# Optimization experiments

Hardware: AMD Instinct MI355X
Metric: run time of the kernel (lower is better)

Reference implementation:

```python
import jax, jax.numpy as jnp
import numpy as np

N = 8192
E = 524288
D_IN, D_HID, D_OUT = 3, 16, 16


def setup_inputs() -> dict:
    key = jax.random.key(0)
    ks = jax.random.split(key, 9)
    node_feats = jax.random.normal(ks[0], (N, D_IN), dtype=jnp.float32)
    edge_idx = jax.random.randint(ks[1], (2, E), 0, N, dtype=jnp.int64)
    # GIN epsilon (train_eps=True -> learned scalar, init 0)
    eps = jnp.zeros((), dtype=jnp.float32)
    # MLP params (Kaiming-uniform-ish scale)
    def lin(k, fan_in, fan_out):
        lim = 1.0 / np.sqrt(fan_in)
        kw, kb = jax.random.split(k)
        W = jax.random.uniform(kw, (fan_in, fan_out), minval=-lim, maxval=lim, dtype=jnp.float32)
        b = jax.random.uniform(kb, (fan_out,), minval=-lim, maxval=lim, dtype=jnp.float32)
        return W, b
    W1, b1 = lin(ks[2], D_IN, D_HID)
    W2, b2 = lin(ks[3], D_HID, D_OUT)
    W3, b3 = lin(ks[4], D_OUT, 1)
    return {"node_feats": node_feats, "edge_idx": edge_idx, "eps": eps,
            "W1": W1, "b1": b1, "W2": W2, "b2": b2, "W3": W3, "b3": b3}


def reference(node_feats, edge_idx, eps, W1, b1, W2, b2, W3, b3):
    src, dst = edge_idx[0], edge_idx[1]
    # GIN aggregation: sum over incoming neighbor features (scatter-add at dst)
    agg = jax.ops.segment_sum(node_feats[src], dst, num_segments=N)  # [N, D_IN]
    z = (1.0 + eps) * node_feats + agg
    # 3-layer MLP with ReLU after every Linear
    h = jax.nn.relu(z @ W1 + b1)
    h = jax.nn.relu(h @ W2 + b2)
    h = jax.nn.relu(h @ W3 + b3)  # [N, 1]
    # outer product: [N,1] @ [1,N] -> [N,N]
    edge_feats = h @ h.T
    return edge_feats
```

## Files before the change

### kernel.cpp

```cpp
#include <hip/hip_runtime.h>
#include <hip/hip_bf16.h>

#define NN 8192
#define EE 524288
#define D_IN 3
#define D_HID 16
#define D_OUT 16
#define NAGG (NN * D_IN)
#define SLICES 64
#define QSPLIT 4
#define EPS_SLICE (EE / SLICES)
#define NODES_Q (NN / QSPLIT)
#define LELE (NODES_Q * D_IN)
#define NCHUNK 8

typedef float f32x4 __attribute__((ext_vector_type(4)));

__device__ __forceinline__ float mlp_eval(float z0, float z1, float z2,
        const float* __restrict__ W1, const float* __restrict__ b1,
        const float* __restrict__ W2, const float* __restrict__ b2,
        const float* __restrict__ W3, const float* __restrict__ b3) {
    float h1[D_HID];
#pragma unroll
    for (int j = 0; j < D_HID; ++j) {
        float v = b1[j] + z0 * W1[0 * D_HID + j] + z1 * W1[1 * D_HID + j] + z2 * W1[2 * D_HID + j];
        h1[j] = v > 0.0f ? v : 0.0f;
    }
    float h2[D_OUT];
#pragma unroll
    for (int j = 0; j < D_OUT; ++j) {
        float v = b2[j];
#pragma unroll
        for (int k = 0; k < D_HID; ++k) v += h1[k] * W2[k * D_OUT + j];
        h2[j] = v > 0.0f ? v : 0.0f;
    }
    float v = b3[0];
#pragma unroll
    for (int k = 0; k < D_OUT; ++k) v += h2[k] * W3[k];
    return v > 0.0f ? v : 0.0f;
}

__global__ __launch_bounds__(512) void scatter_priv_kernel(
        const float* __restrict__ nf,
        const int* __restrict__ eidx,
        float* __restrict__ partials) {
    __shared__ float lagg[LELE];
    const int tid = threadIdx.x;
    const int slice = blockIdx.x & (SLICES - 1);
    const int q = blockIdx.x >> 6;
    for (int i = tid; i < LELE; i += 512) lagg[i] = 0.0f;
    __syncthreads();

    const int base = slice * EPS_SLICE;
    const int nlo = q * NODES_Q;
    for (int e = base + tid; e < base + EPS_SLICE; e += 512) {
        int d = eidx[EE + e];
        unsigned dq = (unsigned)(d - nlo);
        if (dq < (unsigned)NODES_Q) {
            int s = eidx[e];
            atomicAdd(&lagg[dq * 3 + 0], nf[s * 3 + 0]);
            atomicAdd(&lagg[dq * 3 + 1], nf[s * 3 + 1]);
            atomicAdd(&lagg[dq * 3 + 2], nf[s * 3 + 2]);
        }
    }
    __syncthreads();

    f32x4* __restrict__ dst = (f32x4*)(partials + (size_t)slice * NAGG + (size_t)nlo * D_IN);
    const f32x4* __restrict__ src = (const f32x4*)lagg;
    for (int i = tid; i < LELE / 4; i += 512) dst[i] = src[i];
}

__global__ __launch_bounds__(256) void reduce_kernel(
        const float* __restrict__ partials,
        float* __restrict__ partials2) {
    const int c4 = blockIdx.x * 256 + threadIdx.x;
    const int chunk = blockIdx.y;
    const f32x4* __restrict__ p = (const f32x4*)partials;
    f32x4 s = {0.0f, 0.0f, 0.0f, 0.0f};
#pragma unroll
    for (int k = 0; k < SLICES / NCHUNK; ++k)
        s += p[(size_t)(chunk * (SLICES / NCHUNK) + k) * (NAGG / 4) + c4];
    ((f32x4*)partials2)[(size_t)chunk * (NAGG / 4) + c4] = s;
}

__global__ __launch_bounds__(256) void mlp_final_kernel(
        const float* __restrict__ partials2,
        const float* __restrict__ nf,
        const float* __restrict__ epsp,
        const float* __restrict__ W1, const float* __restrict__ b1,
        const float* __restrict__ W2, const float* __restrict__ b2,
        const float* __restrict__ W3, const float* __restrict__ b3,
        float* __restrict__ h) {
    int i = blockIdx.x * blockDim.x + threadIdx.x;
    if (i >= NN) return;
    float z[D_IN];
#pragma unroll
    for (int c = 0; c < D_IN; ++c) {
        float s = 0.0f;
#pragma unroll
        for (int k = 0; k < NCHUNK; ++k) s += partials2[(size_t)k * NAGG + i * 3 + c];
        z[c] = s;
    }
    float eps1 = 1.0f + epsp[0];
    float z0 = eps1 * nf[i * 3 + 0] + z[0];
    float z1 = eps1 * nf[i * 3 + 1] + z[1];
    float z2 = eps1 * nf[i * 3 + 2] + z[2];
    h[i] = mlp_eval(z0, z1, z2, W1, b1, W2, b2, W3, b3);
}

__global__ void zero_agg_kernel(float* __restrict__ agg, int n) {
    int i = blockIdx.x * blockDim.x + threadIdx.x;
    if (i < n) agg[i] = 0.0f;
}

__global__ void scatter_atomic_kernel(const float* __restrict__ nf,
                                      const int* __restrict__ eidx,
                                      float* __restrict__ agg) {
    int e = blockIdx.x * blockDim.x + threadIdx.x;
    if (e >= EE) return;
    int s = eidx[e];
    int d = eidx[EE + e];
    atomicAdd(&agg[d * 3 + 0], nf[s * 3 + 0]);
    atomicAdd(&agg[d * 3 + 1], nf[s * 3 + 1]);
    atomicAdd(&agg[d * 3 + 2], nf[s * 3 + 2]);
}

__global__ void mlp_kernel(const float* __restrict__ nf,
                           const float* __restrict__ agg,
                           const float* __restrict__ epsp,
                           const float* __restrict__ W1, const float* __restrict__ b1,
                           const float* __restrict__ W2, const float* __restrict__ b2,
                           const float* __restrict__ W3, const float* __restrict__ b3,
                           float* __restrict__ h) {
    int i = blockIdx.x * blockDim.x + threadIdx.x;
    if (i >= NN) return;
    float eps1 = 1.0f + epsp[0];
    float z0 = eps1 * nf[i * 3 + 0] + agg[i * 3 + 0];
    float z1 = eps1 * nf[i * 3 + 1] + agg[i * 3 + 1];
    float z2 = eps1 * nf[i * 3 + 2] + agg[i * 3 + 2];
    h[i] = mlp_eval(z0, z1, z2, W1, b1, W2, b2, W3, b3);
}

__global__ __launch_bounds__(256) void outer_kernel(const float* __restrict__ h,
                                                    float4* __restrict__ out) {
    int i = blockIdx.x;
    float hi = h[i];
    const float4* __restrict__ h4 = reinterpret_cast<const float4*>(h);
    float4* __restrict__ row = out + (size_t)i * (NN / 4);
#pragma unroll 4
    for (int j = threadIdx.x; j < NN / 4; j += 256) {
        float4 v = h4[j];
        float4 o;
        o.x = hi * v.x; o.y = hi * v.y; o.z = hi * v.z; o.w = hi * v.w;
        row[j] = o;
    }
}

extern "C" void kernel_launch(void* const* d_in, const int* in_sizes, int n_in,
                              void* d_out, int out_size, void* d_ws, size_t ws_size,
                              hipStream_t stream) {
    const float* nf   = (const float*)d_in[0];
    const int*   eidx = (const int*)d_in[1];
    const float* eps  = (const float*)d_in[2];
    const float* W1   = (const float*)d_in[3];
    const float* b1   = (const float*)d_in[4];
    const float* W2   = (const float*)d_in[5];
    const float* b2   = (const float*)d_in[6];
    const float* W3   = (const float*)d_in[7];
    const float* b3   = (const float*)d_in[8];
    float* out = (float*)d_out;

    float* h         = (float*)d_ws;
    float* agg       = h + NN;
    float* partials2 = agg + NAGG;
    float* partials  = partials2 + (size_t)NCHUNK * NAGG;

    size_t need = (size_t)(NN + NAGG + (size_t)NCHUNK * NAGG + (size_t)SLICES * NAGG) * sizeof(float);

    if (ws_size >= need) {
        scatter_priv_kernel<<<SLICES * QSPLIT, 512, 0, stream>>>(nf, eidx, partials);
        dim3 rgrid(NAGG / 4 / 256, NCHUNK);
        reduce_kernel<<<rgrid, 256, 0, stream>>>(partials, partials2);
        mlp_final_kernel<<<NN / 256, 256, 0, stream>>>(partials2, nf, eps, W1, b1, W2, b2, W3, b3, h);
    } else {
        zero_agg_kernel<<<(NAGG + 255) / 256, 256, 0, stream>>>(agg, NAGG);
        scatter_atomic_kernel<<<(EE + 255) / 256, 256, 0, stream>>>(nf, eidx, agg);
        mlp_kernel<<<(NN + 255) / 256, 256, 0, stream>>>(nf, agg, eps, W1, b1, W2, b2, W3, b3, h);
    }
    outer_kernel<<<NN, 256, 0, stream>>>(h, (float4*)out);
}
```

Before: 68.50 us.

## Fuse partial reduction into MLP kernel and widen outer-product rows per block

Replaces the two-stage reduction (reduce_kernel into partials2, then mlp_final_kernel) with one kernel. Each block sums all 64 slice partials for its 256 nodes into shared memory and then evaluates the MLP, which removes one launch and the partials2 round trip. The outer-product kernel now writes 8 rows per 512-thread block and reuses each loaded h vector across those rows, cutting block count and redundant loads of h. The fused reduction runs on only 32 blocks with 192 active reducer threads each, so that stage has much less parallelism than before.

```diff
diff --git a/kernel.cpp b/kernel.cpp
--- a/kernel.cpp
+++ b/kernel.cpp
@@ -12,7 +12,8 @@
 #define EPS_SLICE (EE / SLICES)
 #define NODES_Q (NN / QSPLIT)
 #define LELE (NODES_Q * D_IN)
-#define NCHUNK 8
+#define ROWS_PER_BLK 8
+#define OUTER_THREADS 512
 
 typedef float f32x4 __attribute__((ext_vector_type(4)));
 
@@ -70,42 +71,34 @@
     for (int i = tid; i < LELE / 4; i += 512) dst[i] = src[i];
 }
 
-__global__ __launch_bounds__(256) void reduce_kernel(
+__global__ __launch_bounds__(256) void reduce_mlp_fused_kernel(
         const float* __restrict__ partials,
-        float* __restrict__ partials2) {
-    const int c4 = blockIdx.x * 256 + threadIdx.x;
-    const int chunk = blockIdx.y;
-    const f32x4* __restrict__ p = (const f32x4*)partials;
-    f32x4 s = {0.0f, 0.0f, 0.0f, 0.0f};
-#pragma unroll
-    for (int k = 0; k < SLICES / NCHUNK; ++k)
-        s += p[(size_t)(chunk * (SLICES / NCHUNK) + k) * (NAGG / 4) + c4];
-    ((f32x4*)partials2)[(size_t)chunk * (NAGG / 4) + c4] = s;
-}
-
-__global__ __launch_bounds__(256) void mlp_final_kernel(
-        const float* __restrict__ partials2,
         const float* __restrict__ nf,
         const float* __restrict__ epsp,
         const float* __restrict__ W1, const float* __restrict__ b1,
         const float* __restrict__ W2, const float* __restrict__ b2,
         const float* __restrict__ W3, const float* __restrict__ b3,
         float* __restrict__ h) {
-    int i = blockIdx.x * blockDim.x + threadIdx.x;
-    if (i >= NN) return;
-    float z[D_IN];
-#pragma unroll
-    for (int c = 0; c < D_IN; ++c) {
-        float s = 0.0f;
-#pragma unroll
-        for (int k = 0; k < NCHUNK; ++k) s += partials2[(size_t)k * NAGG + i * 3 + c];
-        z[c] = s;
+    __shared__ f32x4 lz[192];
+    const int t = threadIdx.x;
+    if (t < 192) {
+        const f32x4* __restrict__ p = (const f32x4*)partials;
+        const int c4 = blockIdx.x * 192 + t;
+        f32x4 s = {0.0f, 0.0f, 0.0f, 0.0f};
+#pragma unroll 8
+        for (int k = 0; k < SLICES; ++k)
+            s += p[(size_t)k * (NAGG / 4) + c4];
+        lz[t] = s;
     }
-    float eps1 = 1.0f + epsp[0];
-    float z0 = eps1 * nf[i * 3 + 0] + z[0];
-    float z1 = eps1 * nf[i * 3 + 1] + z[1];
-    float z2 = eps1 * nf[i * 3 + 2] + z[2];
-    h[i] = mlp_eval(z0, z1, z2, W1, b1, W2, b2, W3, b3);
+    __syncthreads();
+
+    const int node = blockIdx.x * 256 + t;
+    const float* __restrict__ l = (const float*)lz;
+    const float eps1 = 1.0f + epsp[0];
+    float z0 = eps1 * nf[node * 3 + 0] + l[t * 3 + 0];
+    float z1 = eps1 * nf[node * 3 + 1] + l[t * 3 + 1];
+    float z2 = eps1 * nf[node * 3 + 2] + l[t * 3 + 2];
+    h[node] = mlp_eval(z0, z1, z2, W1, b1, W2, b2, W3, b3);
 }
 
 __global__ void zero_agg_kernel(float* __restrict__ agg, int n) {
@@ -141,18 +134,20 @@
     h[i] = mlp_eval(z0, z1, z2, W1, b1, W2, b2, W3, b3);
 }
 
-__global__ __launch_bounds__(256) void outer_kernel(const float* __restrict__ h,
-                                                    float4* __restrict__ out) {
-    int i = blockIdx.x;
-    float hi = h[i];
-    const float4* __restrict__ h4 = reinterpret_cast<const float4*>(h);
-    float4* __restrict__ row = out + (size_t)i * (NN / 4);
+__global__ __launch_bounds__(OUTER_THREADS) void outer_kernel(
+        const float* __restrict__ h, f32x4* __restrict__ out) {
+    const int r0 = blockIdx.x * ROWS_PER_BLK;
+    float hi[ROWS_PER_BLK];
+#pragma unroll
+    for (int r = 0; r < ROWS_PER_BLK; ++r) hi[r] = h[r0 + r];
+    const f32x4* __restrict__ h4 = (const f32x4*)h;
+    f32x4* __restrict__ base = out + (size_t)r0 * (NN / 4);
 #pragma unroll 4
-    for (int j = threadIdx.x; j < NN / 4; j += 256) {
-        float4 v = h4[j];
-        float4 o;
-        o.x = hi * v.x; o.y = hi * v.y; o.z = hi * v.z; o.w = hi * v.w;
-        row[j] = o;
+    for (int j = threadIdx.x; j < NN / 4; j += OUTER_THREADS) {
+        f32x4 v = h4[j];
+#pragma unroll
+        for (int r = 0; r < ROWS_PER_BLK; ++r)
+            base[(size_t)r * (NN / 4) + j] = v * hi[r];
     }
 }
 
@@ -170,22 +165,20 @@
     const float* b3   = (const float*)d_in[8];
     float* out = (float*)d_out;
 
-    float* h         = (float*)d_ws;
-    float* agg       = h + NN;
-    float* partials2 = agg + NAGG;
-    float* partials  = partials2 + (size_t)NCHUNK * NAGG;
+    float* h        = (float*)d_ws;
+    float* agg      = h + NN;
+    float* partials = agg + NAGG;
 
-    size_t need = (size_t)(NN + NAGG + (size_t)NCHUNK * NAGG + (size_t)SLICES * NAGG) * sizeof(float);
+    size_t need = (size_t)(NN + NAGG + (size_t)SLICES * NAGG) * sizeof(float);
 
     if (ws_size >= need) {
         scatter_priv_kernel<<<SLICES * QSPLIT, 512, 0, stream>>>(nf, eidx, partials);
-        dim3 rgrid(NAGG / 4 / 256, NCHUNK);
-        reduce_kernel<<<rgrid, 256, 0, stream>>>(partials, partials2);
-        mlp_final_kernel<<<NN / 256, 256, 0, stream>>>(partials2, nf, eps, W1, b1, W2, b2, W3, b3, h);
+        reduce_mlp_fused_kernel<<<NN / 256, 256, 0, stream>>>(
+            partials, nf, eps, W1, b1, W2, b2, W3, b3, h);
     } else {
         zero_agg_kernel<<<(NAGG + 255) / 256, 256, 0, stream>>>(agg, NAGG);
         scatter_atomic_kernel<<<(EE + 255) / 256, 256, 0, stream>>>(nf, eidx, agg);
         mlp_kernel<<<(NN + 255) / 256, 256, 0, stream>>>(nf, agg, eps, W1, b1, W2, b2, W3, b3, h);
     }
-    outer_kernel<<<NN, 256, 0, stream>>>(h, (float4*)out);
+    outer_kernel<<<NN / ROWS_PER_BLK, OUTER_THREADS, 0, stream>>>(h, (f32x4*)out);
 }
```

Result: slower. 71.54 us (+4.4%).
